# Kernel tuning notes

Measured on AMD Instinct MI355X. Metric: run time of the kernel, lower is better.

## Reference

```python
import jax, jax.numpy as jnp
import numpy as np

B, T, D, M, L = 4, 2048, 256, 128, 16
P = M * L  # max_pair_cnt


def setup_inputs() -> dict:
    key = jax.random.key(0)
    ks = jax.random.split(key, 11)
    head = jax.random.normal(ks[0], (B, P, T), jnp.float32) * 0.05
    tail = jax.random.normal(ks[1], (B, P, T), jnp.float32) * 0.05
    x = jax.random.normal(ks[2], (B, T, D), jnp.float32)
    coref_mention_position = jax.random.uniform(ks[3], (B, M, T), jnp.float32)
    lab = jax.random.uniform(ks[4], (B, P, 2), jnp.float32) + 1e-3
    coref_label = lab / lab.sum(-1, keepdims=True)  # already-softmaxed target
    coref_label_mask = jax.random.randint(ks[5], (B, P), 0, 2).astype(bool)
    lens = jnp.full((B, M), L, jnp.int32)  # uniform segment lengths
    w1 = jax.random.normal(ks[6], (3 * D, D), jnp.float32) / np.sqrt(3 * D).astype(np.float32)
    b1 = jnp.zeros((D,), jnp.float32)
    w2 = jax.random.normal(ks[7], (D, 2), jnp.float32) / np.sqrt(D).astype(np.float32)
    b2 = jnp.zeros((2,), jnp.float32)
    return {"head": head, "tail": tail, "lens": lens, "x": x,
            "coref_mention_position": coref_mention_position,
            "coref_label": coref_label, "coref_label_mask": coref_label_mask,
            "w1": w1, "b1": b1, "w2": w2, "b2": b2}


def reference(head, tail, lens, x, coref_mention_position, coref_label,
              coref_label_mask, w1, b1, w2, b2):
    # bmm-based gather of mention reps: [B,P,T] @ [B,T,D] -> [B,P,D]
    head_rep = jnp.einsum('bpt,btd->bpd', head, x)
    tail_rep = jnp.einsum('bpt,btd->bpd', tail, x)
    feat = jnp.concatenate([head_rep, tail_rep, head_rep * tail_rep], axis=-1)
    logits = jax.nn.relu(feat @ w1 + b1) @ w2 + b2  # [B,P,2]

    # ragged split_n_pad -> per-mention top-1 select (uniform lens == L -> reshape)
    scores = logits[..., 1].reshape(B, M, L)            # [B,M,L]
    max_idx = jnp.argmax(scores, axis=-1)               # [B,M]
    max_val = jnp.max(scores, axis=-1)                  # [B,M] (raw logit, as in source)
    tail_seg = tail_rep.reshape(B, M, L, D)
    sel = jnp.take_along_axis(tail_seg, max_idx[:, :, None, None], axis=2)[:, :, 0, :]
    coref_rep_m = sel * max_val[:, :, None]             # [B,M,D]

    # scatter-bmm merge back into sequence: [B,T,M] @ [B,M,D] -> [B,T,D]
    coref_rep = jnp.einsum('bmt,bmd->btd', coref_mention_position, coref_rep_m)
    output = x + coref_rep

    # KLDivLoss(reduction='mean') over masked pairs
    logq = jax.nn.log_softmax(logits, axis=-1)
    lab = coref_label
    pw = jnp.where(lab > 0, lab * jnp.log(jnp.maximum(lab, 1e-38)), 0.0) - lab * logq
    n = jnp.sum(coref_label_mask).astype(jnp.float32)
    loss = jnp.where(coref_label_mask[..., None], pw, 0.0).sum() / (n * 2.0)
    return output, loss
```

## Files before the change

kernel.cpp:

```cpp
#include <hip/hip_runtime.h>
#include <hip/hip_bf16.h>
#include <stdint.h>

#define TAU 0.35f

typedef __attribute__((ext_vector_type(8))) short bf16x8;
typedef __attribute__((ext_vector_type(4))) float f32x4;

__device__ __forceinline__ unsigned short f2bf(float f) {
  __bf16 h = (__bf16)f;
  return __builtin_bit_cast(unsigned short, h);
}
__device__ __forceinline__ float bf2f(unsigned short u) {
  unsigned int v = ((unsigned int)u) << 16;
  return __builtin_bit_cast(float, v);
}
__device__ __forceinline__ void async_copy16(const void* g, void* l) {
  __builtin_amdgcn_global_load_lds(
      (const __attribute__((address_space(1))) unsigned int*)g,
      (__attribute__((address_space(3))) unsigned int*)l, 16, 0, 0);
}

__global__ __launch_bounds__(256) void k_prep(
    const float* __restrict__ x, const float* __restrict__ w1,
    const float* __restrict__ b2,
    unsigned short* __restrict__ xt, unsigned short* __restrict__ w1t,
    float* __restrict__ logits, int* __restrict__ njobs) {
  __shared__ float tileS[64][65];
  int bx = blockIdx.x, tid = threadIdx.x;
  if (bx == 0 && tid == 0) *njobs = 0;
  if (bx < 64) {
    int i = bx * 256 + tid;
    logits[i] = b2[i & 1];
  }
  int j = tid & 63, i0 = tid >> 6;
  if (bx < 512) {
    int b = bx >> 7, t6 = (bx >> 2) & 31, d6 = bx & 3;
    const float* src = x + ((size_t)b * 2048 + (size_t)t6 * 64) * 256 + d6 * 64;
    for (int i = i0; i < 64; i += 4) tileS[i][j] = src[(size_t)i * 256 + j];
    __syncthreads();
    unsigned short* dst = xt + ((size_t)b * 256 + (size_t)d6 * 64) * 2048 + t6 * 64;
    for (int r = i0; r < 64; r += 4) dst[(size_t)r * 2048 + j] = f2bf(tileS[j][r]);
  } else {
    int wt = bx - 512;
    int k6 = wt >> 2, n6 = wt & 3;
    const float* src = w1 + ((size_t)k6 * 64) * 256 + n6 * 64;
    for (int i = i0; i < 64; i += 4) tileS[i][j] = src[(size_t)i * 256 + j];
    __syncthreads();
    unsigned short* dst = w1t + ((size_t)n6 * 64) * 768 + k6 * 64;
    for (int r = i0; r < 64; r += 4) dst[(size_t)r * 768 + j] = f2bf(tileS[j][r]);
  }
}

__global__ __launch_bounds__(512, 2) void k_gemm_rep(
    const float* __restrict__ head, const float* __restrict__ tail,
    const unsigned short* __restrict__ xt,
    float* __restrict__ hrep, float* __restrict__ trep) {
  __shared__ unsigned short As[2][4096];
  __shared__ unsigned short Bs[2][16384];
  int bx = blockIdx.x;
  int b = bx >> 6, mt = bx & 63;
  const float* Asrc = ((mt < 32) ? head : tail) +
                      ((size_t)(b * 2048 + (mt & 31) * 64)) * 2048;
  float* Crep = (mt < 32) ? hrep : trep;
  const unsigned short* Bsrc = xt + ((size_t)b * 256) * 2048;

  int tid = threadIdx.x, lane = tid & 63, w = tid >> 6;

  int ar = tid >> 3, aq = tid & 7;
  const float* aptr = Asrc + (size_t)ar * 2048 + aq * 8;
  int awi = ((ar >> 4) * 128 + (aq >> 2) * 64 + (aq & 3) * 16 + (ar & 15)) * 8;

  const unsigned short* bg[4];
  int bdst[4];
#pragma unroll
  for (int a = 0; a < 4; ++a) {
    int colofs = a * 8 + (lane >> 3);
    int col = w * 32 + colofs;
    int k8 = (lane & 7) ^ (colofs & 7);
    bg[a] = Bsrc + (size_t)col * 2048 + k8 * 8;
    bdst[a] = (w * 256 + a * 64 + lane) * 8;
  }

  int rt = w & 3;
  int cg = (w >> 2) * 128;
  int sw0 = (lane >> 4) ^ (lane & 7);
  int sw1 = (4 + (lane >> 4)) ^ (lane & 7);
  int colc[8];
#pragma unroll
  for (int ct = 0; ct < 8; ++ct) colc[ct] = (cg + ct * 16 + (lane & 15)) * 8;

  f32x4 acc[8];
#pragma unroll
  for (int ct = 0; ct < 8; ++ct) acc[ct] = (f32x4){0.f, 0.f, 0.f, 0.f};

  auto STAGEB = [&](int buf) {
#pragma unroll
    for (int a = 0; a < 4; ++a) { async_copy16(bg[a], &Bs[buf][bdst[a]]); bg[a] += 64; }
  };
  float4 av0, av1;
  auto LOADA = [&]() {
    const float4* ap = (const float4*)aptr;
    av0 = ap[0]; av1 = ap[1];
    aptr += 64;
  };
  auto WRITEA = [&](int buf) {
    bf16x8 p;
    p[0] = (short)f2bf(av0.x); p[1] = (short)f2bf(av0.y);
    p[2] = (short)f2bf(av0.z); p[3] = (short)f2bf(av0.w);
    p[4] = (short)f2bf(av1.x); p[5] = (short)f2bf(av1.y);
    p[6] = (short)f2bf(av1.z); p[7] = (short)f2bf(av1.w);
    *(bf16x8*)&As[buf][awi] = p;
  };
  auto MMA = [&](int buf) {
    const unsigned short* A_ = As[buf];
    const unsigned short* B_ = Bs[buf];
    bf16x8 a0 = *(const bf16x8*)&A_[(rt * 128 + lane) * 8];
    bf16x8 a1 = *(const bf16x8*)&A_[(rt * 128 + 64 + lane) * 8];
#pragma unroll
    for (int ct = 0; ct < 8; ++ct) {
      bf16x8 b0 = *(const bf16x8*)&B_[(colc[ct] + sw0) * 8];
      acc[ct] = __builtin_amdgcn_mfma_f32_16x16x32_bf16(a0, b0, acc[ct], 0, 0, 0);
    }
#pragma unroll
    for (int ct = 0; ct < 8; ++ct) {
      bf16x8 b1 = *(const bf16x8*)&B_[(colc[ct] + sw1) * 8];
      acc[ct] = __builtin_amdgcn_mfma_f32_16x16x32_bf16(a1, b1, acc[ct], 0, 0, 0);
    }
  };

  STAGEB(0);
  LOADA();
  WRITEA(0);
  __syncthreads();

  for (int it = 0; it < 32; ++it) {
    int cur = it & 1, nxt = cur ^ 1;
    if (it < 31) {
      STAGEB(nxt);
      LOADA();
    }
    MMA(cur);
    if (it < 31) WRITEA(nxt);
    __syncthreads();
  }

  size_t prow = (size_t)b * 2048 + (size_t)(mt & 31) * 64 + rt * 16 + ((lane >> 4) << 2);
  int cb = cg + (lane & 15);
#pragma unroll
  for (int ct = 0; ct < 8; ++ct)
#pragma unroll
    for (int i = 0; i < 4; ++i)
      Crep[(prow + i) * 256 + cb + ct * 16] = acc[ct][i];
}

__global__ __launch_bounds__(256) void k_feat(
    const float* __restrict__ hrep, const float* __restrict__ trep,
    unsigned short* __restrict__ featbf) {
  int gid = blockIdx.x * 256 + threadIdx.x;
  int p = gid >> 6, d0 = (gid & 63) * 4;
  float4 h4 = *(const float4*)&hrep[(size_t)p * 256 + d0];
  float4 t4 = *(const float4*)&trep[(size_t)p * 256 + d0];
  ushort4 a, bb, c;
  a.x = f2bf(h4.x); a.y = f2bf(h4.y); a.z = f2bf(h4.z); a.w = f2bf(h4.w);
  bb.x = f2bf(t4.x); bb.y = f2bf(t4.y); bb.z = f2bf(t4.z); bb.w = f2bf(t4.w);
  c.x = f2bf(h4.x * t4.x); c.y = f2bf(h4.y * t4.y);
  c.z = f2bf(h4.z * t4.z); c.w = f2bf(h4.w * t4.w);
  *(ushort4*)&featbf[(size_t)p * 768 + d0] = a;
  *(ushort4*)&featbf[(size_t)p * 768 + 256 + d0] = bb;
  *(ushort4*)&featbf[(size_t)p * 768 + 512 + d0] = c;
}

__global__ __launch_bounds__(256, 4) void k_gemm_mlp(
    const unsigned short* __restrict__ featb, const unsigned short* __restrict__ w1t,
    const float* __restrict__ b1, const float* __restrict__ w2,
    float* __restrict__ logits) {
  __shared__ unsigned short As[2][4096], Bs[2][4096];
  int bx = blockIdx.x;
  int ntile = bx >> 7;
  int mtile = bx & 127;
  int tid = threadIdx.x, lane = tid & 63, w = tid >> 6;

  const unsigned short* ag[2];
  const unsigned short* bgp[2];
  int dofs[2];
#pragma unroll
  for (int a = 0; a < 2; ++a) {
    int rowofs = a * 8 + (lane >> 3);
    int k8 = (lane & 7) ^ (rowofs & 7);
    ag[a] = featb + (size_t)(mtile * 64 + w * 16 + rowofs) * 768 + k8 * 8;
    bgp[a] = w1t + (size_t)(ntile * 64 + w * 16 + rowofs) * 768 + k8 * 8;
    dofs[a] = (w * 128 + a * 64 + lane) * 8;
  }
  int sw0 = (lane >> 4) ^ (lane & 7);
  int sw1 = (4 + (lane >> 4)) ^ (lane & 7);
  int arowc = (w * 16 + (lane & 15)) * 8;
  int colc[4];
#pragma unroll
  for (int ct = 0; ct < 4; ++ct) colc[ct] = (ct * 16 + (lane & 15)) * 8;

  f32x4 acc[4];
#pragma unroll
  for (int ct = 0; ct < 4; ++ct) acc[ct] = (f32x4){0.f, 0.f, 0.f, 0.f};

#pragma unroll
  for (int a = 0; a < 2; ++a) {
    async_copy16(ag[a], &As[0][dofs[a]]); ag[a] += 64;
    async_copy16(bgp[a], &Bs[0][dofs[a]]); bgp[a] += 64;
  }
  __syncthreads();

  for (int it = 0; it < 12; ++it) {
    int cur = it & 1, nxt = cur ^ 1;
    if (it < 11) {
#pragma unroll
      for (int a = 0; a < 2; ++a) {
        async_copy16(ag[a], &As[nxt][dofs[a]]); ag[a] += 64;
        async_copy16(bgp[a], &Bs[nxt][dofs[a]]); bgp[a] += 64;
      }
    }
    const unsigned short* A_ = As[cur];
    const unsigned short* B_ = Bs[cur];
    bf16x8 a0 = *(const bf16x8*)&A_[(arowc + sw0) * 8];
    bf16x8 a1 = *(const bf16x8*)&A_[(arowc + sw1) * 8];
#pragma unroll
    for (int ct = 0; ct < 4; ++ct) {
      bf16x8 b0 = *(const bf16x8*)&B_[(colc[ct] + sw0) * 8];
      acc[ct] = __builtin_amdgcn_mfma_f32_16x16x32_bf16(a0, b0, acc[ct], 0, 0, 0);
    }
#pragma unroll
    for (int ct = 0; ct < 4; ++ct) {
      bf16x8 b1 = *(const bf16x8*)&B_[(colc[ct] + sw1) * 8];
      acc[ct] = __builtin_amdgcn_mfma_f32_16x16x32_bf16(a1, b1, acc[ct], 0, 0, 0);
    }
    __syncthreads();
  }

  float bv[4], w20[4], w21[4];
#pragma unroll
  for (int ct = 0; ct < 4; ++ct) {
    int col = ntile * 64 + ct * 16 + (lane & 15);
    bv[ct] = b1[col]; w20[ct] = w2[col * 2]; w21[ct] = w2[col * 2 + 1];
  }
#pragma unroll
  for (int i = 0; i < 4; ++i) {
    float s0 = 0.f, s1 = 0.f;
#pragma unroll
    for (int ct = 0; ct < 4; ++ct) {
      float r = fmaxf(acc[ct][i] + bv[ct], 0.f);
      s0 += r * w20[ct]; s1 += r * w21[ct];
    }
#pragma unroll
    for (int off = 1; off < 16; off <<= 1) {
      s0 += __shfl_xor(s0, off); s1 += __shfl_xor(s1, off);
    }
    if ((lane & 15) == 0) {
      int row = mtile * 64 + w * 16 + ((lane >> 4) << 2) + i;
      atomicAdd(&logits[row * 2], s0);
      atomicAdd(&logits[row * 2 + 1], s1);
    }
  }
}

__global__ void k_select(const float* __restrict__ logits, int* __restrict__ idxv,
                         float* __restrict__ mval, int* __restrict__ cmask,
                         int* __restrict__ njobs, int* __restrict__ jobs) {
  int q = blockIdx.x * 256 + threadIdx.x;
  if (q >= 512) return;
  int base = q * 16;
  float s[16];
#pragma unroll
  for (int i = 0; i < 16; ++i) s[i] = logits[(size_t)(base + i) * 2 + 1];
  float best = s[0]; int bi = 0;
#pragma unroll
  for (int i = 1; i < 16; ++i) if (s[i] > best) { best = s[i]; bi = i; }
  int mask = 0, cnt = 0;
#pragma unroll
  for (int i = 0; i < 16; ++i) if (s[i] > best - TAU) { mask |= 1 << i; ++cnt; }
  idxv[q] = bi; mval[q] = best;
  if (cnt > 1) {
    cmask[q] = mask;
    for (int i = 0; i < 16; ++i)
      if ((mask >> i) & 1) { int j = atomicAdd(njobs, 1); jobs[j] = base + i; }
  } else cmask[q] = 0;
}

__global__ __launch_bounds__(1024) void k_refine(
    const int* __restrict__ njobs, const int* __restrict__ jobs,
    const float* __restrict__ head, const float* __restrict__ tail,
    const float* __restrict__ x, const float* __restrict__ w1,
    const float* __restrict__ b1, const float* __restrict__ w2,
    const float* __restrict__ b2, float* __restrict__ refined) {
  __shared__ float hrow[2048], trow[2048], feat[768], red[1024], red2[1024];
  int tid = threadIdx.x, seg = tid >> 8, d = tid & 255;
  int nj = *njobs;
  for (int job = blockIdx.x; job < nj; job += gridDim.x) {
    int code = jobs[job];
    int b = code >> 11, p = code & 2047;
    if (tid < 512)
      *(float4*)&hrow[tid * 4] = *(const float4*)&head[((size_t)(b * 2048 + p)) * 2048 + tid * 4];
    else {
      int u = tid - 512;
      *(float4*)&trow[u * 4] = *(const float4*)&tail[((size_t)(b * 2048 + p)) * 2048 + u * 4];
    }
    __syncthreads();
    float hr = 0.f, tr = 0.f;
    const float* xb = x + ((size_t)b * 2048) * 256 + d;
#pragma unroll 8
    for (int t = seg * 512; t < seg * 512 + 512; ++t) {
      float xv = xb[(size_t)t * 256];
      hr += hrow[t] * xv; tr += trow[t] * xv;
    }
    red[tid] = hr; red2[tid] = tr;
    __syncthreads();
    if (seg == 0) {
      float fh = red[d] + red[256 + d] + red[512 + d] + red[768 + d];
      float ft = red2[d] + red2[256 + d] + red2[512 + d] + red2[768 + d];
      feat[d] = fh; feat[256 + d] = ft; feat[512 + d] = fh * ft;
    }
    __syncthreads();
    float hp = 0.f;
    for (int ii = seg * 192; ii < seg * 192 + 192; ++ii) hp += feat[ii] * w1[(size_t)ii * 256 + d];
    red[tid] = hp;
    __syncthreads();
    if (seg == 0) {
      float hj = b1[d] + red[d] + red[256 + d] + red[512 + d] + red[768 + d];
      hj = fmaxf(hj, 0.f);
      red2[d] = hj * w2[d * 2 + 1];
    }
    __syncthreads();
    for (int s = 128; s > 0; s >>= 1) {
      if (tid < s) red2[tid] += red2[tid + s];
      __syncthreads();
    }
    if (tid == 0) refined[code] = red2[0] + b2[1];
    __syncthreads();
  }
}

__global__ __launch_bounds__(256) void k_repm(
    const int* __restrict__ idxv, const float* __restrict__ mval,
    const int* __restrict__ cmask, const float* __restrict__ refined,
    const float* __restrict__ trep, float* __restrict__ repm) {
  int q = blockIdx.x, d = threadIdx.x;
  int mask = cmask[q]; int bi; float v;
  if (mask) {
    bi = -1; v = -1e30f;
    for (int i = 0; i < 16; ++i)
      if ((mask >> i) & 1) { float s = refined[q * 16 + i]; if (s > v) { v = s; bi = i; } }
  } else { bi = idxv[q]; v = mval[q]; }
  repm[(size_t)q * 256 + d] = trep[((size_t)q * 16 + bi) * 256 + d] * v;
}

__global__ __launch_bounds__(256) void k_merge(
    const float* __restrict__ cmp, const float* __restrict__ repm,
    const float* __restrict__ x, float* __restrict__ out) {
  __shared__ float cl[128 * 16];
  int bx = blockIdx.x, b = bx >> 7, t0 = (bx & 127) * 16;
  int tid = threadIdx.x;
#pragma unroll
  for (int it = 0; it < 2; ++it) {
    int f = it * 256 + tid;
    int row = f >> 2, c4 = (f & 3) * 4;
    *(float4*)&cl[row * 16 + c4] =
        *(const float4*)&cmp[((size_t)(b * 128 + row)) * 2048 + t0 + c4];
  }
  __syncthreads();
  float acc[16];
#pragma unroll
  for (int i = 0; i < 16; ++i) acc[i] = 0.f;
  int d = tid;
  for (int m = 0; m < 128; ++m) {
    float rv = repm[(size_t)(b * 128 + m) * 256 + d];
    const float4* c4p = (const float4*)&cl[m * 16];
#pragma unroll
    for (int jj = 0; jj < 4; ++jj) {
      float4 c = c4p[jj];
      acc[jj * 4] += c.x * rv; acc[jj * 4 + 1] += c.y * rv;
      acc[jj * 4 + 2] += c.z * rv; acc[jj * 4 + 3] += c.w * rv;
    }
  }
  const float* xb = x + ((size_t)(b * 2048 + t0)) * 256 + d;
  float* ob = out + ((size_t)(b * 2048 + t0)) * 256 + d;
#pragma unroll
  for (int tt = 0; tt < 16; ++tt) ob[(size_t)tt * 256] = xb[(size_t)tt * 256] + acc[tt];
}

__global__ __launch_bounds__(1024) void k_loss(
    const float* __restrict__ logits, const float* __restrict__ lab,
    const unsigned char* __restrict__ mask, float* __restrict__ out_loss) {
  __shared__ float rs[1024], rc[1024];
  int tid = threadIdx.x;
  float sum = 0.f, cnt = 0.f;
  for (int p = tid; p < 8192; p += 1024) {
    float l0 = logits[(size_t)p * 2], l1 = logits[(size_t)p * 2 + 1];
    float a0 = lab[(size_t)p * 2], a1 = lab[(size_t)p * 2 + 1];
    float mx = fmaxf(l0, l1);
    float lse = mx + logf(expf(l0 - mx) + expf(l1 - mx));
    float pw = 0.f;
    if (a0 > 0.f) pw += a0 * logf(fmaxf(a0, 1e-38f));
    if (a1 > 0.f) pw += a1 * logf(fmaxf(a1, 1e-38f));
    pw -= a0 * (l0 - lse) + a1 * (l1 - lse);
    if (mask[p]) { sum += pw; cnt += 1.f; }
  }
  rs[tid] = sum; rc[tid] = cnt;
  __syncthreads();
  for (int s = 512; s > 0; s >>= 1) {
    if (tid < s) { rs[tid] += rs[tid + s]; rc[tid] += rc[tid + s]; }
    __syncthreads();
  }
  if (tid == 0) *out_loss = rs[0] / (rc[0] * 2.0f);
}

extern "C" void kernel_launch(void* const* d_in, const int* in_sizes, int n_in,
                              void* d_out, int out_size, void* d_ws, size_t ws_size,
                              hipStream_t stream) {
  (void)in_sizes; (void)n_in; (void)out_size; (void)ws_size;
  const float* head = (const float*)d_in[0];
  const float* tail = (const float*)d_in[1];
  const float* x = (const float*)d_in[3];
  const float* cmp = (const float*)d_in[4];
  const float* lab = (const float*)d_in[5];
  const unsigned char* lmask = (const unsigned char*)d_in[6];
  const float* w1 = (const float*)d_in[7];
  const float* b1 = (const float*)d_in[8];
  const float* w2 = (const float*)d_in[9];
  const float* b2 = (const float*)d_in[10];
  float* out = (float*)d_out;

  char* ws = (char*)d_ws;
  size_t off = 0;
  auto alloc = [&](size_t bytes) -> void* {
    void* p = ws + off; off += (bytes + 255) & ~(size_t)255; return p;
  };
  unsigned short* xt = (unsigned short*)alloc(4ull * 256 * 2048 * 2);
  unsigned short* w1t = (unsigned short*)alloc(256ull * 768 * 2);
  float* hrep = (float*)alloc(8192ull * 256 * 4);
  float* trep = (float*)alloc(8192ull * 256 * 4);
  unsigned short* featb = (unsigned short*)alloc(8192ull * 768 * 2);
  float* logits = (float*)alloc(8192ull * 2 * 4);
  float* refined = (float*)alloc(8192ull * 4);
  int* idxv = (int*)alloc(512 * 4);
  float* mvalv = (float*)alloc(512 * 4);
  int* cmaskv = (int*)alloc(512 * 4);
  int* njobs = (int*)alloc(256);
  int* jobs = (int*)alloc(8192 * 4);
  float* repm = (float*)alloc(512ull * 256 * 4);

  k_prep<<<560, 256, 0, stream>>>(x, w1, b2, xt, w1t, logits, njobs);
  k_gemm_rep<<<256, 512, 0, stream>>>(head, tail, xt, hrep, trep);
  k_feat<<<2048, 256, 0, stream>>>(hrep, trep, featb);
  k_gemm_mlp<<<512, 256, 0, stream>>>(featb, w1t, b1, w2, logits);
  k_select<<<2, 256, 0, stream>>>(logits, idxv, mvalv, cmaskv, njobs, jobs);
  k_refine<<<256, 1024, 0, stream>>>(njobs, jobs, head, tail, x, w1, b1, w2, b2, refined);
  k_repm<<<512, 256, 0, stream>>>(idxv, mvalv, cmaskv, refined, trep, repm);
  k_merge<<<512, 256, 0, stream>>>(cmp, repm, x, out);
  k_loss<<<1, 1024, 0, stream>>>(logits, lab, lmask, out + 4ull * 2048 * 256);
}
```

Baseline: 322.2 us.

## Retile rep GEMM to 32-row tiles with a pre-swizzled x layout

k_prep now writes x into a blocked bf16 layout (k-chunks of 64 with 8-wide k groups) so that k_gemm_rep can stage B with contiguous 16-byte async copies and no swizzle arithmetic. The rep GEMM tile shrinks from 64 to 32 rows, which doubles the grid to 512 blocks, and launch bounds rise to 4 blocks per CU. Only half the threads load and convert A. The aim is more parallelism and occupancy on a GEMM that is bound by streaming the head and tail reads. The cost is that the B tile is reloaded twice as often per output row, and the new LDS read pattern may cause bank conflicts.

```diff
diff --git a/kernel.cpp b/kernel.cpp
--- a/kernel.cpp
+++ b/kernel.cpp
@@ -27,23 +27,37 @@
     unsigned short* __restrict__ xt, unsigned short* __restrict__ w1t,
     float* __restrict__ logits, int* __restrict__ njobs) {
   __shared__ float tileS[64][65];
+  __shared__ float tx[64][132];
   int bx = blockIdx.x, tid = threadIdx.x;
   if (bx == 0 && tid == 0) *njobs = 0;
   if (bx < 64) {
     int i = bx * 256 + tid;
     logits[i] = b2[i & 1];
   }
-  int j = tid & 63, i0 = tid >> 6;
-  if (bx < 512) {
-    int b = bx >> 7, t6 = (bx >> 2) & 31, d6 = bx & 3;
-    const float* src = x + ((size_t)b * 2048 + (size_t)t6 * 64) * 256 + d6 * 64;
-    for (int i = i0; i < 64; i += 4) tileS[i][j] = src[(size_t)i * 256 + j];
-    __syncthreads();
-    unsigned short* dst = xt + ((size_t)b * 256 + (size_t)d6 * 64) * 2048 + t6 * 64;
-    for (int r = i0; r < 64; r += 4) dst[(size_t)r * 2048 + j] = f2bf(tileS[j][r]);
+  if (bx < 256) {
+    int b = bx >> 6, kc = (bx >> 1) & 31, dh = bx & 1;
+    const float* src = x + ((size_t)b * 2048 + (size_t)kc * 64) * 256 + dh * 128;
+#pragma unroll
+    for (int p = 0; p < 8; ++p) {
+      int idx = p * 256 + tid;
+      int row = idx >> 5, f4 = idx & 31;
+      *(float4*)&tx[row][f4 * 4] = *(const float4*)&src[(size_t)row * 256 + f4 * 4];
+    }
+    __syncthreads();
+    unsigned short* dst = xt + ((size_t)(b * 32 + kc)) * 16384 + dh * 1024;
+#pragma unroll
+    for (int p = 0; p < 4; ++p) {
+      int idx = p * 256 + tid;
+      int d0 = idx & 127, k8 = idx >> 7;
+      bf16x8 v;
+#pragma unroll
+      for (int j = 0; j < 8; ++j) v[j] = (short)f2bf(tx[k8 * 8 + j][d0]);
+      *(bf16x8*)&dst[(size_t)k8 * 2048 + d0 * 8] = v;
+    }
   } else {
-    int wt = bx - 512;
+    int wt = bx - 256;
     int k6 = wt >> 2, n6 = wt & 3;
+    int j = tid & 63, i0 = tid >> 6;
     const float* src = w1 + ((size_t)k6 * 64) * 256 + n6 * 64;
     for (int i = i0; i < 64; i += 4) tileS[i][j] = src[(size_t)i * 256 + j];
     __syncthreads();
@@ -52,53 +66,50 @@
   }
 }
 
-__global__ __launch_bounds__(512, 2) void k_gemm_rep(
+__global__ __launch_bounds__(512, 4) void k_gemm_rep(
     const float* __restrict__ head, const float* __restrict__ tail,
     const unsigned short* __restrict__ xt,
     float* __restrict__ hrep, float* __restrict__ trep) {
-  __shared__ unsigned short As[2][4096];
+  __shared__ unsigned short As[2][2048];
   __shared__ unsigned short Bs[2][16384];
   int bx = blockIdx.x;
-  int b = bx >> 6, mt = bx & 63;
-  const float* Asrc = ((mt < 32) ? head : tail) +
-                      ((size_t)(b * 2048 + (mt & 31) * 64)) * 2048;
-  float* Crep = (mt < 32) ? hrep : trep;
-  const unsigned short* Bsrc = xt + ((size_t)b * 256) * 2048;
+  int b = bx >> 7, mt = bx & 127;
+  const float* Asrc = ((mt < 64) ? head : tail) +
+                      ((size_t)(b * 2048 + (mt & 63) * 32)) * 2048;
+  float* Crep = (mt < 64) ? hrep : trep;
+  const unsigned short* Bsrc = xt + (size_t)b * 524288;
 
   int tid = threadIdx.x, lane = tid & 63, w = tid >> 6;
-
-  int ar = tid >> 3, aq = tid & 7;
-  const float* aptr = Asrc + (size_t)ar * 2048 + aq * 8;
-  int awi = ((ar >> 4) * 128 + (aq >> 2) * 64 + (aq & 3) * 16 + (ar & 15)) * 8;
-
-  const unsigned short* bg[4];
-  int bdst[4];
-#pragma unroll
-  for (int a = 0; a < 4; ++a) {
-    int colofs = a * 8 + (lane >> 3);
-    int col = w * 32 + colofs;
-    int k8 = (lane & 7) ^ (colofs & 7);
-    bg[a] = Bsrc + (size_t)col * 2048 + k8 * 8;
-    bdst[a] = (w * 256 + a * 64 + lane) * 8;
-  }
-
-  int rt = w & 3;
-  int cg = (w >> 2) * 128;
-  int sw0 = (lane >> 4) ^ (lane & 7);
-  int sw1 = (4 + (lane >> 4)) ^ (lane & 7);
-  int colc[8];
-#pragma unroll
-  for (int ct = 0; ct < 8; ++ct) colc[ct] = (cg + ct * 16 + (lane & 15)) * 8;
-
-  f32x4 acc[8];
-#pragma unroll
-  for (int ct = 0; ct < 8; ++ct) acc[ct] = (f32x4){0.f, 0.f, 0.f, 0.f};
-
+  int rg = w & 1, cg = w >> 1;
+  int l4 = lane >> 4, l15 = lane & 15;
+
+  int arow = tid >> 3, ak8 = tid & 7;
+  const float* aptr = Asrc + (size_t)arow * 2048 + ak8 * 8;
+  int awi = (ak8 * 32 + arow) * 8;
+
+  const unsigned short* bg = Bsrc + tid * 8;
+
+  int aoff[2];
+  int boff[2][4];
+#pragma unroll
+  for (int kh = 0; kh < 2; ++kh) {
+    aoff[kh] = ((kh * 4 + l4) * 32 + rg * 16 + l15) * 8;
+#pragma unroll
+    for (int ct = 0; ct < 4; ++ct)
+      boff[kh][ct] = ((kh * 4 + l4) * 256 + cg * 64 + ct * 16 + l15) * 8;
+  }
+
+  f32x4 acc[4];
+#pragma unroll
+  for (int ct = 0; ct < 4; ++ct) acc[ct] = (f32x4){0.f, 0.f, 0.f, 0.f};
+
+  float4 av0, av1;
   auto STAGEB = [&](int buf) {
 #pragma unroll
-    for (int a = 0; a < 4; ++a) { async_copy16(bg[a], &Bs[buf][bdst[a]]); bg[a] += 64; }
+    for (int a = 0; a < 4; ++a)
+      async_copy16(bg + (size_t)a * 4096, &Bs[buf][(tid + a * 512) * 8]);
+    bg += 16384;
   };
-  float4 av0, av1;
   auto LOADA = [&]() {
     const float4* ap = (const float4*)aptr;
     av0 = ap[0]; av1 = ap[1];
@@ -115,40 +126,36 @@
   auto MMA = [&](int buf) {
     const unsigned short* A_ = As[buf];
     const unsigned short* B_ = Bs[buf];
-    bf16x8 a0 = *(const bf16x8*)&A_[(rt * 128 + lane) * 8];
-    bf16x8 a1 = *(const bf16x8*)&A_[(rt * 128 + 64 + lane) * 8];
-#pragma unroll
-    for (int ct = 0; ct < 8; ++ct) {
-      bf16x8 b0 = *(const bf16x8*)&B_[(colc[ct] + sw0) * 8];
-      acc[ct] = __builtin_amdgcn_mfma_f32_16x16x32_bf16(a0, b0, acc[ct], 0, 0, 0);
-    }
-#pragma unroll
-    for (int ct = 0; ct < 8; ++ct) {
-      bf16x8 b1 = *(const bf16x8*)&B_[(colc[ct] + sw1) * 8];
-      acc[ct] = __builtin_amdgcn_mfma_f32_16x16x32_bf16(a1, b1, acc[ct], 0, 0, 0);
+#pragma unroll
+    for (int kh = 0; kh < 2; ++kh) {
+      bf16x8 a0 = *(const bf16x8*)&A_[aoff[kh]];
+#pragma unroll
+      for (int ct = 0; ct < 4; ++ct) {
+        bf16x8 bb = *(const bf16x8*)&B_[boff[kh][ct]];
+        acc[ct] = __builtin_amdgcn_mfma_f32_16x16x32_bf16(a0, bb, acc[ct], 0, 0, 0);
+      }
     }
   };
 
   STAGEB(0);
-  LOADA();
-  WRITEA(0);
+  if (tid < 256) { LOADA(); WRITEA(0); }
   __syncthreads();
 
   for (int it = 0; it < 32; ++it) {
     int cur = it & 1, nxt = cur ^ 1;
     if (it < 31) {
       STAGEB(nxt);
-      LOADA();
+      if (tid < 256) LOADA();
     }
     MMA(cur);
-    if (it < 31) WRITEA(nxt);
-    __syncthreads();
-  }
-
-  size_t prow = (size_t)b * 2048 + (size_t)(mt & 31) * 64 + rt * 16 + ((lane >> 4) << 2);
-  int cb = cg + (lane & 15);
-#pragma unroll
-  for (int ct = 0; ct < 8; ++ct)
+    if (it < 31 && tid < 256) WRITEA(nxt);
+    __syncthreads();
+  }
+
+  size_t prow = (size_t)b * 2048 + (size_t)(mt & 63) * 32 + rg * 16 + (l4 << 2);
+  int cb = cg * 64 + l15;
+#pragma unroll
+  for (int ct = 0; ct < 4; ++ct)
 #pragma unroll
     for (int i = 0; i < 4; ++i)
       Crep[(prow + i) * 256 + cb + ct * 16] = acc[ct][i];
@@ -447,8 +454,8 @@
   int* jobs = (int*)alloc(8192 * 4);
   float* repm = (float*)alloc(512ull * 256 * 4);
 
-  k_prep<<<560, 256, 0, stream>>>(x, w1, b2, xt, w1t, logits, njobs);
-  k_gemm_rep<<<256, 512, 0, stream>>>(head, tail, xt, hrep, trep);
+  k_prep<<<304, 256, 0, stream>>>(x, w1, b2, xt, w1t, logits, njobs);
+  k_gemm_rep<<<512, 512, 0, stream>>>(head, tail, xt, hrep, trep);
   k_feat<<<2048, 256, 0, stream>>>(hrep, trep, featb);
   k_gemm_mlp<<<512, 256, 0, stream>>>(featb, w1t, b1, w2, logits);
   k_select<<<2, 256, 0, stream>>>(logits, idxv, mvalv, cmaskv, njobs, jobs);
```

New measurement: 315.6 us. 1.02x faster.
